# Optimization experiments

Hardware: AMD Instinct MI355X
Metric: run time of the kernel (lower is better)

Reference implementation:

```python
import jax, jax.numpy as jnp
import numpy as np

H = 8
D_MODEL = 512
D_K = D_MODEL // H
NEG = -1e9


def setup_inputs() -> dict:
    key = jax.random.key(0)
    ks = jax.random.split(key, 12)
    N, Lq, Lk = 2, 4096, 4096
    inp = {
        "query": jax.random.normal(ks[0], (N, Lq, D_MODEL), dtype=jnp.float32),
        "key": jax.random.normal(ks[1], (N, Lk, D_MODEL), dtype=jnp.float32),
        "value": jax.random.normal(ks[2], (N, Lk, D_MODEL), dtype=jnp.float32),
        "mask": jnp.ones((N, 1, Lk), dtype=jnp.int32),
    }
    scale = 0.02
    for i, nm in enumerate(["q", "k", "v", "o"]):
        inp[f"W{nm}"] = scale * jax.random.normal(ks[3 + i], (D_MODEL, D_MODEL), dtype=jnp.float32)
        inp[f"b{nm}"] = jnp.zeros((D_MODEL,), dtype=jnp.float32)
    return inp


def reference(query, key, value, mask, Wq, bq, Wk, bk, Wv, bv, Wo, bo):
    # torch Linear: y = x @ W.T + b
    N, Lq, _ = query.shape
    Lk = key.shape[1]
    q = (query @ Wq.T + bq).reshape(N, Lq, H, D_K)   # (N,Lq,h,dk)
    k = (key @ Wk.T + bk).reshape(N, Lk, H, D_K)     # (N,Lk,h,dk)
    v = (value @ Wv.T + bv).reshape(N, Lk, H, D_K)   # (N,Lk,h,dk)
    # scores: (N,h,Lq,Lk)
    scores = jnp.einsum("bqhd,bkhd->bhqk", q, k) / jnp.sqrt(jnp.float32(D_K))
    # mask (N,1,Lk) or (N,Lq,Lk) -> broadcast over heads (and Lq if singleton)
    m = mask[:, None, :, :]  # (N,1,1|Lq,Lk)
    scores = jnp.where(m == 0, jnp.float32(NEG), scores)
    attn = jax.nn.softmax(scores, axis=-1)
    # dropout is identity in eval mode (deterministic reference)
    out = jnp.einsum("bhqk,bkhd->bqhd", attn, v).reshape(N, Lq, D_MODEL)
    return out @ Wo.T + bo
```

## Files before the change

### kernel.cpp

```cpp
#include <hip/hip_runtime.h>
#include <hip/hip_bf16.h>

#define H 8
#define DM 512
#define DK 64
#define LSEQ 4096
#define NB 2
#define NSPLIT 4
#define KSPAN (LSEQ / NSPLIT)
#define NIT (KSPAN / 64)

#define QSCALE 0.18033688011112042f

typedef float f32x4 __attribute__((ext_vector_type(4)));
typedef __bf16 bf16x8 __attribute__((ext_vector_type(8)));
typedef __bf16 bf16x2 __attribute__((ext_vector_type(2)));
typedef unsigned short u16;

__device__ __forceinline__ u16 f2bf(float f) {
    union { float f; unsigned u; } v{f};
    return (u16)((v.u + 0x8000u) >> 16);
}

__device__ __forceinline__ unsigned pkbf(float a, float b) {
#if __has_builtin(__builtin_amdgcn_cvt_pk_bf16_f32)
    union { bf16x2 v; unsigned u; } x;
    x.v = __builtin_amdgcn_cvt_pk_bf16_f32(a, b);
    return x.u;
#else
    union { float f; unsigned u; } x{a}, y{b};
    return ((x.u + 0x8000u) >> 16) | ((y.u + 0x8000u) & 0xffff0000u);
#endif
}

__device__ __forceinline__ ushort4 cvt4(float4 a) {
    union { ushort4 s; uint2 u; } o;
    o.u.x = pkbf(a.x, a.y);
    o.u.y = pkbf(a.z, a.w);
    return o.s;
}

__device__ __forceinline__ float2 ubf2(unsigned u) {
    union { float f; unsigned v; } a, b;
    a.v = u << 16;
    b.v = u & 0xffff0000u;
    return make_float2(a.f, b.f);
}

__device__ __forceinline__ float fexp2(float x) {
#if __has_builtin(__builtin_amdgcn_exp2f)
    return __builtin_amdgcn_exp2f(x);
#else
    return exp2f(x);
#endif
}

__device__ __forceinline__ f32x4 mfma32(bf16x8 a, bf16x8 b, f32x4 c) {
    return __builtin_amdgcn_mfma_f32_16x16x32_bf16(a, b, c, 0, 0, 0);
}

__launch_bounds__(256, 2)
__global__ void proj_qkv(const float* __restrict__ Xq, const float* __restrict__ Xk,
                         const float* __restrict__ Xv,
                         const float* __restrict__ Wq, const float* __restrict__ Wk,
                         const float* __restrict__ Wv,
                         const float* __restrict__ bq, const float* __restrict__ bk,
                         const float* __restrict__ bv,
                         const int* __restrict__ mask,
                         u16* __restrict__ qo, u16* __restrict__ ko, u16* __restrict__ vo)
{
    const int mode = blockIdx.z;
    const float* X    = (mode == 0) ? Xq : (mode == 1) ? Xk : Xv;
    const float* W    = (mode == 0) ? Wq : (mode == 1) ? Wk : Wv;
    const float* bias = (mode == 0) ? bq : (mode == 1) ? bk : bv;
    u16* out          = (mode == 0) ? qo : (mode == 1) ? ko : vo;

    __shared__ __align__(16) u16 As[2][128][72];
    __shared__ __align__(16) u16 Bs[2][128][72];

    const int tid  = threadIdx.x;
    const int wave = tid >> 6;
    const int lane = tid & 63;
    const int g    = lane >> 4;
    const int ln   = lane & 15;
    const int wr   = wave >> 1;
    const int wc   = wave & 1;

    const int m0 = blockIdx.x * 128;
    const int n0 = blockIdx.y * 128;

    float4 xa[8], wb[8];
    #pragma unroll
    for (int i = 0; i < 8; ++i) {
        int idx = tid + 256 * i;
        int row = idx >> 4;
        int col = (idx & 15) * 4;
        xa[i] = *(const float4*)(X + (size_t)(m0 + row) * DM + col);
        wb[i] = *(const float4*)(W + (size_t)(n0 + row) * DM + col);
    }
    #pragma unroll
    for (int i = 0; i < 8; ++i) {
        int idx = tid + 256 * i;
        int row = idx >> 4;
        int col = (idx & 15) * 4;
        *(ushort4*)&As[0][row][col] = cvt4(xa[i]);
        *(ushort4*)&Bs[0][row][col] = cvt4(wb[i]);
    }

    f32x4 acc[4][4] = {};

    for (int kt = 0; kt < 8; ++kt) {
        const int cur = kt & 1;
        __syncthreads();

        if (kt < 7) {
            int kb = (kt + 1) * 64;
            #pragma unroll
            for (int i = 0; i < 8; ++i) {
                int idx = tid + 256 * i;
                int row = idx >> 4;
                int col = (idx & 15) * 4;
                xa[i] = *(const float4*)(X + (size_t)(m0 + row) * DM + kb + col);
                wb[i] = *(const float4*)(W + (size_t)(n0 + row) * DM + kb + col);
            }
        }

        bf16x8 af[4][2], bf[4][2];
        #pragma unroll
        for (int t = 0; t < 4; ++t) {
            af[t][0] = *(const bf16x8*)&As[cur][wr * 64 + t * 16 + ln][g * 8];
            af[t][1] = *(const bf16x8*)&As[cur][wr * 64 + t * 16 + ln][32 + g * 8];
            bf[t][0] = *(const bf16x8*)&Bs[cur][wc * 64 + t * 16 + ln][g * 8];
            bf[t][1] = *(const bf16x8*)&Bs[cur][wc * 64 + t * 16 + ln][32 + g * 8];
        }
        #pragma unroll
        for (int mt = 0; mt < 4; ++mt)
            #pragma unroll
            for (int nt = 0; nt < 4; ++nt) {
                acc[mt][nt] = mfma32(af[mt][0], bf[nt][0], acc[mt][nt]);
                acc[mt][nt] = mfma32(af[mt][1], bf[nt][1], acc[mt][nt]);
            }

        if (kt < 7) {
            int nxt = 1 - cur;
            #pragma unroll
            for (int i = 0; i < 8; ++i) {
                int idx = tid + 256 * i;
                int row = idx >> 4;
                int col = (idx & 15) * 4;
                *(ushort4*)&As[nxt][row][col] = cvt4(xa[i]);
                *(ushort4*)&Bs[nxt][row][col] = cvt4(wb[i]);
            }
        }
    }

    if (mode != 2) {
        #pragma unroll
        for (int nt = 0; nt < 4; ++nt) {
            int n  = n0 + wc * 64 + nt * 16 + ln;
            float bias_n = bias[n];
            int hh = n >> 6;
            int d  = n & (DK - 1);
            #pragma unroll
            for (int mt = 0; mt < 4; ++mt)
                #pragma unroll
                for (int r = 0; r < 4; ++r) {
                    int m  = m0 + wr * 64 + mt * 16 + g * 4 + r;
                    int bb = m >> 12;
                    int s  = m & (LSEQ - 1);
                    float val = acc[mt][nt][r] + bias_n;
                    if (mode == 0) val *= QSCALE;
                    else           val = mask[bb * LSEQ + s] ? val : 0.0f;
                    out[(size_t)((bb * H + hh) * LSEQ + s) * DK + d] = f2bf(val);
                }
        }
    } else {
        __syncthreads();
        u16* Ts = &As[0][0][0];
        const int bb = m0 >> 12;
        const int s0 = m0 & (LSEQ - 1);
        #pragma unroll
        for (int nt = 0; nt < 4; ++nt) {
            int dl = wc * 64 + nt * 16 + ln;
            float bias_n = bias[n0 + dl];
            #pragma unroll
            for (int mt = 0; mt < 4; ++mt)
                #pragma unroll
                for (int r = 0; r < 4; ++r) {
                    int sl = wr * 64 + mt * 16 + g * 4 + r;
                    float val = acc[mt][nt][r] + bias_n;
                    val = mask[bb * LSEQ + s0 + sl] ? val : 0.0f;
                    Ts[dl * 136 + sl] = f2bf(val);
                }
        }
        __syncthreads();
        int dl   = tid >> 1;
        int half = tid & 1;
        int n  = n0 + dl;
        int hh = n >> 6;
        int d  = n & (DK - 1);
        int sb = s0 + half * 64;
        u16* dst = out + ((size_t)((bb * H + hh) * DK + d) * LSEQ + sb);
        const u16* srcp = Ts + dl * 136 + half * 64;
        #pragma unroll
        for (int i = 0; i < 8; ++i)
            *(uint4*)(dst + i * 8) = *(const uint4*)(srcp + i * 8);
    }
}

__launch_bounds__(256, 4)
__global__ void flash(const u16* __restrict__ qws, const u16* __restrict__ kws,
                      const u16* __restrict__ vws, const int* __restrict__ mask,
                      u16* __restrict__ Opart, float* __restrict__ lpart)
{
    __shared__ u16 Ks[2][64][64];
    __shared__ u16 Vs[2][64][64];

    const int tid   = threadIdx.x;
    const int wave  = tid >> 6;
    const int lane  = tid & 63;
    const int g     = lane >> 4;
    const int ln    = lane & 15;
    const int b     = blockIdx.z;
    const int h     = blockIdx.y;
    const int qblk  = blockIdx.x & 31;
    const int split = blockIdx.x >> 5;
    const int q0    = qblk * 128;
    const int kstart = split * KSPAN;

    const u16* qp = qws + ((size_t)((b * H + h) * LSEQ) + q0 + wave * 32 + ln) * DK;
    const u16* kp = kws + (size_t)(b * H + h) * LSEQ * DK;
    const u16* vp = vws + (size_t)(b * H + h) * DK * LSEQ;
    const int* mp = mask + b * LSEQ;

    int nmask = 0;
    for (int t = 0; t < NIT; ++t) {
        int mval = mp[kstart + t * 64 + lane];
        unsigned long long bal = __ballot(mval == 0);
        nmask += (int)__popcll(bal);
    }
    const float fnmask = (float)nmask;

    bf16x8 qf[2][2];
    qf[0][0] = *(const bf16x8*)(qp + g * 8);
    qf[0][1] = *(const bf16x8*)(qp + 32 + g * 8);
    qf[1][0] = *(const bf16x8*)(qp + 16 * DK + g * 8);
    qf[1][1] = *(const bf16x8*)(qp + 16 * DK + 32 + g * 8);

    union OU { unsigned u[4]; bf16x8 v; } onesu;
    onesu.u[0] = onesu.u[1] = onesu.u[2] = onesu.u[3] = 0x3F803F80u;
    const bf16x8 vones = onesu.v;

    f32x4 accO[2][4] = {};
    f32x4 accL[2] = {};
    const f32x4 fzero = {};

    const int row = tid >> 3;
    const int c   = tid & 7;
    const int swz = row & 7;
    const int kcol = (c ^ swz) * 8;
    const int vcol0 = ((2 * c) & 3) * 16 + (c >> 1) * 4;
    const int vs0 = vcol0 >> 3;
    const int vof = vcol0 & 7;
    const int vw0 = ((vs0 ^ swz) * 8) + vof;
    const int vw1 = (((vs0 + 2) ^ swz) * 8) + vof;
    const int rs = ln & 7;

    uint4 kr0, kr1, vr0, vr1;
    kr0 = *(const uint4*)(kp + (size_t)(kstart + row) * DK + c * 8);
    kr1 = *(const uint4*)(kp + (size_t)(kstart + row + 32) * DK + c * 8);
    vr0 = *(const uint4*)(vp + (size_t)row * LSEQ + kstart + c * 8);
    vr1 = *(const uint4*)(vp + (size_t)(row + 32) * LSEQ + kstart + c * 8);
    *(uint4*)&Ks[0][row][kcol]      = kr0;
    *(uint4*)&Ks[0][row + 32][kcol] = kr1;
    *(uint2*)&Vs[0][row][vw0]       = make_uint2(vr0.x, vr0.y);
    *(uint2*)&Vs[0][row][vw1]       = make_uint2(vr0.z, vr0.w);
    *(uint2*)&Vs[0][row + 32][vw0]  = make_uint2(vr1.x, vr1.y);
    *(uint2*)&Vs[0][row + 32][vw1]  = make_uint2(vr1.z, vr1.w);

    for (int it = 0; it < NIT; ++it) {
        const int cur = it & 1;
        __syncthreads();

        if (it < NIT - 1) {
            int kn = kstart + it * 64 + 64;
            kr0 = *(const uint4*)(kp + (size_t)(kn + row) * DK + c * 8);
            kr1 = *(const uint4*)(kp + (size_t)(kn + row + 32) * DK + c * 8);
            vr0 = *(const uint4*)(vp + (size_t)row * LSEQ + kn + c * 8);
            vr1 = *(const uint4*)(vp + (size_t)(row + 32) * LSEQ + kn + c * 8);
        }

        __builtin_amdgcn_s_setprio(1);
        f32x4 sc[2][4];
        #pragma unroll
        for (int kb = 0; kb < 4; ++kb) {
            bf16x8 kf0 = *(const bf16x8*)&Ks[cur][kb * 16 + ln][(g ^ rs) * 8];
            bf16x8 kf1 = *(const bf16x8*)&Ks[cur][kb * 16 + ln][((g + 4) ^ rs) * 8];
            #pragma unroll
            for (int j = 0; j < 2; ++j) {
                f32x4 z = mfma32(kf0, qf[j][0], fzero);
                z = mfma32(kf1, qf[j][1], z);
                sc[j][kb] = z;
            }
        }
        __builtin_amdgcn_s_setprio(0);

        #pragma unroll
        for (int kb = 0; kb < 4; ++kb)
            #pragma unroll
            for (int j = 0; j < 2; ++j) {
                sc[j][kb][0] = fexp2(sc[j][kb][0]);
                sc[j][kb][1] = fexp2(sc[j][kb][1]);
                sc[j][kb][2] = fexp2(sc[j][kb][2]);
                sc[j][kb][3] = fexp2(sc[j][kb][3]);
            }

        union PU { unsigned u[4]; bf16x8 v; } p01[2], p23[2];
        #pragma unroll
        for (int j = 0; j < 2; ++j) {
            p01[j].u[0] = pkbf(sc[j][0][0], sc[j][0][1]);
            p01[j].u[1] = pkbf(sc[j][0][2], sc[j][0][3]);
            p01[j].u[2] = pkbf(sc[j][1][0], sc[j][1][1]);
            p01[j].u[3] = pkbf(sc[j][1][2], sc[j][1][3]);
            p23[j].u[0] = pkbf(sc[j][2][0], sc[j][2][1]);
            p23[j].u[1] = pkbf(sc[j][2][2], sc[j][2][3]);
            p23[j].u[2] = pkbf(sc[j][3][0], sc[j][3][1]);
            p23[j].u[3] = pkbf(sc[j][3][2], sc[j][3][3]);
        }

        __builtin_amdgcn_s_setprio(1);
        #pragma unroll
        for (int j = 0; j < 2; ++j) {
            accL[j] = mfma32(p01[j].v, vones, accL[j]);
            accL[j] = mfma32(p23[j].v, vones, accL[j]);
        }
        #pragma unroll
        for (int t = 0; t < 4; ++t) {
            bf16x8 vb01 = *(const bf16x8*)&Vs[cur][t * 16 + ln][((2 * g) ^ rs) * 8];
            bf16x8 vb23 = *(const bf16x8*)&Vs[cur][t * 16 + ln][((2 * g + 1) ^ rs) * 8];
            #pragma unroll
            for (int j = 0; j < 2; ++j) {
                accO[j][t] = mfma32(p01[j].v, vb01, accO[j][t]);
                accO[j][t] = mfma32(p23[j].v, vb23, accO[j][t]);
            }
        }
        __builtin_amdgcn_s_setprio(0);

        if (it < NIT - 1) {
            int nxt = 1 - cur;
            *(uint4*)&Ks[nxt][row][kcol]      = kr0;
            *(uint4*)&Ks[nxt][row + 32][kcol] = kr1;
            *(uint2*)&Vs[nxt][row][vw0]       = make_uint2(vr0.x, vr0.y);
            *(uint2*)&Vs[nxt][row][vw1]       = make_uint2(vr0.z, vr0.w);
            *(uint2*)&Vs[nxt][row + 32][vw0]  = make_uint2(vr1.x, vr1.y);
            *(uint2*)&Vs[nxt][row + 32][vw1]  = make_uint2(vr1.z, vr1.w);
        }
    }

    const size_t PLANE = (size_t)NB * LSEQ * DM;
    u16* opp = Opart + (size_t)split * PLANE;

    #pragma unroll
    for (int j = 0; j < 2; ++j) {
        if (ln == 0) {
            #pragma unroll
            for (int r = 0; r < 4; ++r)
                lpart[(size_t)split * (NB * H * LSEQ) + ((size_t)(b * H + h) * LSEQ)
                      + q0 + wave * 32 + j * 16 + g * 4 + r] = accL[j][r] - fnmask;
        }
        #pragma unroll
        for (int r = 0; r < 4; ++r) {
            float linv = 1.0f / (accL[j][r] - fnmask);
            size_t base = ((size_t)(b * LSEQ) + q0 + wave * 32 + j * 16 + g * 4 + r) * DM + h * DK;
            #pragma unroll
            for (int t = 0; t < 4; ++t)
                opp[base + t * 16 + ln] = f2bf(accO[j][t][r] * linv);
        }
    }
}

__launch_bounds__(256, 4)
__global__ void reduce_split(const u16* __restrict__ Opart, const float* __restrict__ lpart,
                             u16* __restrict__ ows)
{
    const size_t PLANE = (size_t)NB * LSEQ * DM;
    const size_t LP    = (size_t)NB * H * LSEQ;
    size_t gid  = (size_t)blockIdx.x * 256 + threadIdx.x;
    size_t flat = gid * 8;

    int b   = (int)(flat >> 21);
    int rem = (int)(flat & ((1 << 21) - 1));
    int q   = rem >> 9;
    int hh  = (rem & 511) >> 6;
    size_t lidx = ((size_t)(b * H + hh) * LSEQ) + q;

    float ls[NSPLIT];
    float lsum = 0.0f;
    #pragma unroll
    for (int s = 0; s < NSPLIT; ++s) {
        ls[s] = lpart[(size_t)s * LP + lidx];
        lsum += ls[s];
    }
    float inv = 1.0f / lsum;

    float o[8] = {};
    #pragma unroll
    for (int s = 0; s < NSPLIT; ++s) {
        float w = ls[s] * inv;
        uint4 cc = *(const uint4*)(Opart + (size_t)s * PLANE + flat);
        float2 a;
        a = ubf2(cc.x); o[0] += w * a.x; o[1] += w * a.y;
        a = ubf2(cc.y); o[2] += w * a.x; o[3] += w * a.y;
        a = ubf2(cc.z); o[4] += w * a.x; o[5] += w * a.y;
        a = ubf2(cc.w); o[6] += w * a.x; o[7] += w * a.y;
    }
    uint4 r;
    r.x = pkbf(o[0], o[1]);
    r.y = pkbf(o[2], o[3]);
    r.z = pkbf(o[4], o[5]);
    r.w = pkbf(o[6], o[7]);
    *(uint4*)(ows + flat) = r;
}

__launch_bounds__(256, 3)
__global__ void proj_out(const u16* __restrict__ A, const float* __restrict__ Wo,
                         const float* __restrict__ bo, float* __restrict__ out)
{
    __shared__ __align__(16) u16 As[2][128][68];
    __shared__ __align__(16) u16 Bs[2][64][68];

    const int tid  = threadIdx.x;
    const int wave = tid >> 6;
    const int lane = tid & 63;
    const int g    = lane >> 4;
    const int ln   = lane & 15;

    const int m0 = blockIdx.x * 128;
    const int n0 = blockIdx.y * 64;

    uint4 aa[4];
    float4 wb[4];
    #pragma unroll
    for (int i = 0; i < 4; ++i) {
        int idx = tid + 256 * i;
        int row = idx >> 3;
        int col = (idx & 7) * 8;
        aa[i] = *(const uint4*)(A + (size_t)(m0 + row) * DM + col);
        int rwb = idx >> 4;
        int cwb = (idx & 15) * 4;
        wb[i] = *(const float4*)(Wo + (size_t)(n0 + rwb) * DM + cwb);
    }
    #pragma unroll
    for (int i = 0; i < 4; ++i) {
        int idx = tid + 256 * i;
        int row = idx >> 3;
        int col = (idx & 7) * 8;
        *(uint4*)&As[0][row][col] = aa[i];
        int rwb = idx >> 4;
        int cwb = (idx & 15) * 4;
        *(ushort4*)&Bs[0][rwb][cwb] = cvt4(wb[i]);
    }

    f32x4 acc[2][4] = {};

    for (int kt = 0; kt < 8; ++kt) {
        const int cur = kt & 1;
        __syncthreads();

        if (kt < 7) {
            int kb = (kt + 1) * 64;
            #pragma unroll
            for (int i = 0; i < 4; ++i) {
                int idx = tid + 256 * i;
                int row = idx >> 3;
                int col = (idx & 7) * 8;
                aa[i] = *(const uint4*)(A + (size_t)(m0 + row) * DM + kb + col);
                int rwb = idx >> 4;
                int cwb = (idx & 15) * 4;
                wb[i] = *(const float4*)(Wo + (size_t)(n0 + rwb) * DM + kb + cwb);
            }
        }

        bf16x8 af[2][2], bf[4][2];
        #pragma unroll
        for (int mt = 0; mt < 2; ++mt) {
            af[mt][0] = *(const bf16x8*)&As[cur][wave * 32 + mt * 16 + ln][g * 8];
            af[mt][1] = *(const bf16x8*)&As[cur][wave * 32 + mt * 16 + ln][32 + g * 8];
        }
        #pragma unroll
        for (int nt = 0; nt < 4; ++nt) {
            bf[nt][0] = *(const bf16x8*)&Bs[cur][nt * 16 + ln][g * 8];
            bf[nt][1] = *(const bf16x8*)&Bs[cur][nt * 16 + ln][32 + g * 8];
        }
        #pragma unroll
        for (int mt = 0; mt < 2; ++mt)
            #pragma unroll
            for (int nt = 0; nt < 4; ++nt) {
                acc[mt][nt] = mfma32(af[mt][0], bf[nt][0], acc[mt][nt]);
                acc[mt][nt] = mfma32(af[mt][1], bf[nt][1], acc[mt][nt]);
            }

        if (kt < 7) {
            int nxt = 1 - cur;
            #pragma unroll
            for (int i = 0; i < 4; ++i) {
                int idx = tid + 256 * i;
                int row = idx >> 3;
                int col = (idx & 7) * 8;
                *(uint4*)&As[nxt][row][col] = aa[i];
                int rwb = idx >> 4;
                int cwb = (idx & 15) * 4;
                *(ushort4*)&Bs[nxt][rwb][cwb] = cvt4(wb[i]);
            }
        }
    }

    #pragma unroll
    for (int nt = 0; nt < 4; ++nt) {
        int n = n0 + nt * 16 + ln;
        float bias_n = bo[n];
        #pragma unroll
        for (int mt = 0; mt < 2; ++mt)
            #pragma unroll
            for (int r = 0; r < 4; ++r) {
                int m = m0 + wave * 32 + mt * 16 + g * 4 + r;
                out[(size_t)m * DM + n] = acc[mt][nt][r] + bias_n;
            }
    }
}

extern "C" void kernel_launch(void* const* d_in, const int* in_sizes, int n_in,
                              void* d_out, int out_size, void* d_ws, size_t ws_size,
                              hipStream_t stream) {
    (void)in_sizes; (void)n_in; (void)out_size; (void)ws_size;

    const float* query = (const float*)d_in[0];
    const float* key   = (const float*)d_in[1];
    const float* value = (const float*)d_in[2];
    const int*   mask  = (const int*)d_in[3];
    const float* Wq = (const float*)d_in[4];
    const float* bq = (const float*)d_in[5];
    const float* Wk = (const float*)d_in[6];
    const float* bk = (const float*)d_in[7];
    const float* Wv = (const float*)d_in[8];
    const float* bv = (const float*)d_in[9];
    const float* Wo = (const float*)d_in[10];
    const float* bo = (const float*)d_in[11];
    float* out = (float*)d_out;

    const size_t PLANE = (size_t)NB * H * LSEQ * DK;
    u16* qws   = (u16*)d_ws;
    u16* kws   = qws + PLANE;
    u16* vws   = kws + PLANE;
    u16* ows   = vws + PLANE;
    u16* Opart = ows + PLANE;
    float* lpart = (float*)(Opart + (size_t)NSPLIT * PLANE);

    dim3 blk(256);
    proj_qkv<<<dim3(64, 4, 3), blk, 0, stream>>>(query, key, value, Wq, Wk, Wv,
                                                 bq, bk, bv, mask, qws, kws, vws);
    flash<<<dim3(32 * NSPLIT, H, NB), blk, 0, stream>>>(qws, kws, vws, mask, Opart, lpart);
    reduce_split<<<dim3(2048), blk, 0, stream>>>(Opart, lpart, ows);
    proj_out<<<dim3(64, 8, 1), blk, 0, stream>>>(ows, Wo, bo, out);
}
```

Before: 231.5 us.

## Fuse split-K softmax combine into output projection A-tile loads

Removes the separate reduce_split kernel and performs the weighted combination of the four partial attention outputs inside proj_out while loading A tiles. This eliminates one kernel launch and the write/read of the intermediate combined buffer. In exchange, each output-projection block re-reads all four partial planes and recomputes the combine, and this is repeated across the column-block grid dimension. The reciprocal is also switched to a fast hardware rcp.

```diff
diff --git a/kernel.cpp b/kernel.cpp
--- a/kernel.cpp
+++ b/kernel.cpp
@@ -45,6 +45,14 @@
     a.v = u << 16;
     b.v = u & 0xffff0000u;
     return make_float2(a.f, b.f);
+}
+
+__device__ __forceinline__ float frcp(float x) {
+#if __has_builtin(__builtin_amdgcn_rcpf)
+    return __builtin_amdgcn_rcpf(x);
+#else
+    return 1.0f / x;
+#endif
 }
 
 __device__ __forceinline__ float fexp2(float x) {
@@ -379,51 +387,59 @@
     }
 }
 
-__launch_bounds__(256, 4)
-__global__ void reduce_split(const u16* __restrict__ Opart, const float* __restrict__ lpart,
-                             u16* __restrict__ ows)
+__device__ __forceinline__ uint4 combine4(const u16* __restrict__ Opart,
+                                          const float* __restrict__ lpart,
+                                          int m, int kcol)
 {
     const size_t PLANE = (size_t)NB * LSEQ * DM;
     const size_t LP    = (size_t)NB * H * LSEQ;
-    size_t gid  = (size_t)blockIdx.x * 256 + threadIdx.x;
-    size_t flat = gid * 8;
-
-    int b   = (int)(flat >> 21);
-    int rem = (int)(flat & ((1 << 21) - 1));
-    int q   = rem >> 9;
-    int hh  = (rem & 511) >> 6;
-    size_t lidx = ((size_t)(b * H + hh) * LSEQ) + q;
-
-    float ls[NSPLIT];
-    float lsum = 0.0f;
-    #pragma unroll
-    for (int s = 0; s < NSPLIT; ++s) {
-        ls[s] = lpart[(size_t)s * LP + lidx];
-        lsum += ls[s];
-    }
-    float inv = 1.0f / lsum;
-
-    float o[8] = {};
-    #pragma unroll
-    for (int s = 0; s < NSPLIT; ++s) {
-        float w = ls[s] * inv;
-        uint4 cc = *(const uint4*)(Opart + (size_t)s * PLANE + flat);
-        float2 a;
-        a = ubf2(cc.x); o[0] += w * a.x; o[1] += w * a.y;
-        a = ubf2(cc.y); o[2] += w * a.x; o[3] += w * a.y;
-        a = ubf2(cc.z); o[4] += w * a.x; o[5] += w * a.y;
-        a = ubf2(cc.w); o[6] += w * a.x; o[7] += w * a.y;
-    }
+    const int b  = m >> 12;
+    const int q  = m & (LSEQ - 1);
+    const int hh = kcol >> 6;
+    const size_t lidx = ((size_t)(b * H + hh) * LSEQ) + q;
+    float l0 = lpart[lidx];
+    float l1 = lpart[LP + lidx];
+    float l2 = lpart[2 * LP + lidx];
+    float l3 = lpart[3 * LP + lidx];
+    float inv = frcp(l0 + l1 + l2 + l3);
+    float w0 = l0 * inv, w1 = l1 * inv, w2 = l2 * inv, w3 = l3 * inv;
+
+    const size_t fi = (size_t)m * DM + kcol;
+    uint4 c0 = *(const uint4*)(Opart + fi);
+    uint4 c1 = *(const uint4*)(Opart + PLANE + fi);
+    uint4 c2 = *(const uint4*)(Opart + 2 * PLANE + fi);
+    uint4 c3 = *(const uint4*)(Opart + 3 * PLANE + fi);
+
+    float o0, o1, o2, o3, o4, o5, o6, o7;
+    float2 a;
+    a = ubf2(c0.x); o0  = w0 * a.x; o1  = w0 * a.y;
+    a = ubf2(c0.y); o2  = w0 * a.x; o3  = w0 * a.y;
+    a = ubf2(c0.z); o4  = w0 * a.x; o5  = w0 * a.y;
+    a = ubf2(c0.w); o6  = w0 * a.x; o7  = w0 * a.y;
+    a = ubf2(c1.x); o0 += w1 * a.x; o1 += w1 * a.y;
+    a = ubf2(c1.y); o2 += w1 * a.x; o3 += w1 * a.y;
+    a = ubf2(c1.z); o4 += w1 * a.x; o5 += w1 * a.y;
+    a = ubf2(c1.w); o6 += w1 * a.x; o7 += w1 * a.y;
+    a = ubf2(c2.x); o0 += w2 * a.x; o1 += w2 * a.y;
+    a = ubf2(c2.y); o2 += w2 * a.x; o3 += w2 * a.y;
+    a = ubf2(c2.z); o4 += w2 * a.x; o5 += w2 * a.y;
+    a = ubf2(c2.w); o6 += w2 * a.x; o7 += w2 * a.y;
+    a = ubf2(c3.x); o0 += w3 * a.x; o1 += w3 * a.y;
+    a = ubf2(c3.y); o2 += w3 * a.x; o3 += w3 * a.y;
+    a = ubf2(c3.z); o4 += w3 * a.x; o5 += w3 * a.y;
+    a = ubf2(c3.w); o6 += w3 * a.x; o7 += w3 * a.y;
+
     uint4 r;
-    r.x = pkbf(o[0], o[1]);
-    r.y = pkbf(o[2], o[3]);
-    r.z = pkbf(o[4], o[5]);
-    r.w = pkbf(o[6], o[7]);
-    *(uint4*)(ows + flat) = r;
+    r.x = pkbf(o0, o1);
+    r.y = pkbf(o2, o3);
+    r.z = pkbf(o4, o5);
+    r.w = pkbf(o6, o7);
+    return r;
 }
 
 __launch_bounds__(256, 3)
-__global__ void proj_out(const u16* __restrict__ A, const float* __restrict__ Wo,
+__global__ void proj_out(const u16* __restrict__ Opart, const float* __restrict__ lpart,
+                         const float* __restrict__ Wo,
                          const float* __restrict__ bo, float* __restrict__ out)
 {
     __shared__ __align__(16) u16 As[2][128][68];
@@ -445,7 +461,7 @@
         int idx = tid + 256 * i;
         int row = idx >> 3;
         int col = (idx & 7) * 8;
-        aa[i] = *(const uint4*)(A + (size_t)(m0 + row) * DM + col);
+        aa[i] = combine4(Opart, lpart, m0 + row, col);
         int rwb = idx >> 4;
         int cwb = (idx & 15) * 4;
         wb[i] = *(const float4*)(Wo + (size_t)(n0 + rwb) * DM + cwb);
@@ -474,7 +490,7 @@
                 int idx = tid + 256 * i;
                 int row = idx >> 3;
                 int col = (idx & 7) * 8;
-                aa[i] = *(const uint4*)(A + (size_t)(m0 + row) * DM + kb + col);
+                aa[i] = combine4(Opart, lpart, m0 + row, kb + col);
                 int rwb = idx >> 4;
                 int cwb = (idx & 15) * 4;
                 wb[i] = *(const float4*)(Wo + (size_t)(n0 + rwb) * DM + kb + cwb);
@@ -560,6 +576,5 @@
     proj_qkv<<<dim3(64, 4, 3), blk, 0, stream>>>(query, key, value, Wq, Wk, Wv,
                                                  bq, bk, bv, mask, qws, kws, vws);
     flash<<<dim3(32 * NSPLIT, H, NB), blk, 0, stream>>>(qws, kws, vws, mask, Opart, lpart);
-    reduce_split<<<dim3(2048), blk, 0, stream>>>(Opart, lpart, ows);
-    proj_out<<<dim3(64, 8, 1), blk, 0, stream>>>(ows, Wo, bo, out);
-}
+    proj_out<<<dim3(64, 8, 1), blk, 0, stream>>>(Opart, lpart, Wo, bo, out);
+}
```

Measured after the change: 255.1 us. 10.2% more time.

## Pre-convert inputs and weights to bf16 in a separate pass, shrink GEMM K-tiles

Applied to the files above, without the earlier changes.

A new cvt_all kernel converts the four weight matrices and the three activation inputs from fp32 to bf16 once, writing them into workspace that reuses the Opart region. proj_qkv and proj_out then load bf16 directly, with K-tile 32 instead of 64, smaller LDS footprints and higher occupancy bounds. The aim is to stop the GEMM tiles from reconverting the same fp32 data many times and to halve their global load volume. The cost is an extra kernel launch plus a full read and write pass over the inputs, and twice as many K-loop iterations and barriers.

```diff
diff --git a/kernel.cpp b/kernel.cpp
--- a/kernel.cpp
+++ b/kernel.cpp
@@ -59,24 +59,51 @@
     return __builtin_amdgcn_mfma_f32_16x16x32_bf16(a, b, c, 0, 0, 0);
 }
 
-__launch_bounds__(256, 2)
-__global__ void proj_qkv(const float* __restrict__ Xq, const float* __restrict__ Xk,
-                         const float* __restrict__ Xv,
-                         const float* __restrict__ Wq, const float* __restrict__ Wk,
-                         const float* __restrict__ Wv,
+__launch_bounds__(256, 8)
+__global__ void cvt_all(const float* __restrict__ W0, const float* __restrict__ W1,
+                        const float* __restrict__ W2, const float* __restrict__ W3,
+                        const float* __restrict__ X0, const float* __restrict__ X1,
+                        const float* __restrict__ X2,
+                        u16* __restrict__ wout, u16* __restrict__ xout)
+{
+    const int y = blockIdx.y;
+    const float* src;
+    u16* dst;
+    int nblk;
+    if (y < 4) {
+        src = (y == 0) ? W0 : (y == 1) ? W1 : (y == 2) ? W2 : W3;
+        dst = wout + (size_t)y * DM * DM;
+        nblk = (DM * DM) / (256 * 8);
+    } else {
+        src = (y == 4) ? X0 : (y == 5) ? X1 : X2;
+        dst = xout + (size_t)(y - 4) * ((size_t)NB * LSEQ * DM);
+        nblk = ((size_t)NB * LSEQ * DM) / (256 * 8);
+    }
+    if ((int)blockIdx.x >= nblk) return;
+    size_t base = ((size_t)blockIdx.x * 256 + threadIdx.x) * 8;
+    float4 a = *(const float4*)(src + base);
+    float4 b = *(const float4*)(src + base + 4);
+    *(ushort4*)(dst + base)     = cvt4(a);
+    *(ushort4*)(dst + base + 4) = cvt4(b);
+}
+
+__launch_bounds__(256, 3)
+__global__ void proj_qkv(const u16* __restrict__ xbf,
+                         const u16* __restrict__ wbf,
                          const float* __restrict__ bq, const float* __restrict__ bk,
                          const float* __restrict__ bv,
                          const int* __restrict__ mask,
                          u16* __restrict__ qo, u16* __restrict__ ko, u16* __restrict__ vo)
 {
     const int mode = blockIdx.z;
-    const float* X    = (mode == 0) ? Xq : (mode == 1) ? Xk : Xv;
-    const float* W    = (mode == 0) ? Wq : (mode == 1) ? Wk : Wv;
+    const u16* X      = xbf + (size_t)mode * ((size_t)NB * LSEQ * DM);
+    const u16* Wb     = wbf + (size_t)mode * DM * DM;
     const float* bias = (mode == 0) ? bq : (mode == 1) ? bk : bv;
     u16* out          = (mode == 0) ? qo : (mode == 1) ? ko : vo;
 
-    __shared__ __align__(16) u16 As[2][128][72];
-    __shared__ __align__(16) u16 Bs[2][128][72];
+    __shared__ __align__(16) u16 sbuf[2][2][128][40];
+    u16 (*As)[128][40] = sbuf[0];
+    u16 (*Bs)[128][40] = sbuf[1];
 
     const int tid  = threadIdx.x;
     const int wave = tid >> 6;
@@ -89,67 +116,63 @@
     const int m0 = blockIdx.x * 128;
     const int n0 = blockIdx.y * 128;
 
-    float4 xa[8], wb[8];
-    #pragma unroll
-    for (int i = 0; i < 8; ++i) {
+    uint4 xa[2], wa[2];
+    #pragma unroll
+    for (int i = 0; i < 2; ++i) {
         int idx = tid + 256 * i;
-        int row = idx >> 4;
-        int col = (idx & 15) * 4;
-        xa[i] = *(const float4*)(X + (size_t)(m0 + row) * DM + col);
-        wb[i] = *(const float4*)(W + (size_t)(n0 + row) * DM + col);
-    }
-    #pragma unroll
-    for (int i = 0; i < 8; ++i) {
+        int row = idx >> 2;
+        int col = (idx & 3) * 8;
+        xa[i] = *(const uint4*)(X  + (size_t)(m0 + row) * DM + col);
+        wa[i] = *(const uint4*)(Wb + (size_t)(n0 + row) * DM + col);
+    }
+    #pragma unroll
+    for (int i = 0; i < 2; ++i) {
         int idx = tid + 256 * i;
-        int row = idx >> 4;
-        int col = (idx & 15) * 4;
-        *(ushort4*)&As[0][row][col] = cvt4(xa[i]);
-        *(ushort4*)&Bs[0][row][col] = cvt4(wb[i]);
+        int row = idx >> 2;
+        int col = (idx & 3) * 8;
+        *(uint4*)&As[0][row][col] = xa[i];
+        *(uint4*)&Bs[0][row][col] = wa[i];
     }
 
     f32x4 acc[4][4] = {};
 
-    for (int kt = 0; kt < 8; ++kt) {
+    for (int kt = 0; kt < 16; ++kt) {
         const int cur = kt & 1;
         __syncthreads();
 
-        if (kt < 7) {
-            int kb = (kt + 1) * 64;
-            #pragma unroll
-            for (int i = 0; i < 8; ++i) {
+        if (kt < 15) {
+            int kb = (kt + 1) * 32;
+            #pragma unroll
+            for (int i = 0; i < 2; ++i) {
                 int idx = tid + 256 * i;
-                int row = idx >> 4;
-                int col = (idx & 15) * 4;
-                xa[i] = *(const float4*)(X + (size_t)(m0 + row) * DM + kb + col);
-                wb[i] = *(const float4*)(W + (size_t)(n0 + row) * DM + kb + col);
-            }
-        }
-
-        bf16x8 af[4][2], bf[4][2];
+                int row = idx >> 2;
+                int col = (idx & 3) * 8;
+                xa[i] = *(const uint4*)(X  + (size_t)(m0 + row) * DM + kb + col);
+                wa[i] = *(const uint4*)(Wb + (size_t)(n0 + row) * DM + kb + col);
+            }
+        }
+
+        bf16x8 af[4], bf[4];
         #pragma unroll
         for (int t = 0; t < 4; ++t) {
-            af[t][0] = *(const bf16x8*)&As[cur][wr * 64 + t * 16 + ln][g * 8];
-            af[t][1] = *(const bf16x8*)&As[cur][wr * 64 + t * 16 + ln][32 + g * 8];
-            bf[t][0] = *(const bf16x8*)&Bs[cur][wc * 64 + t * 16 + ln][g * 8];
-            bf[t][1] = *(const bf16x8*)&Bs[cur][wc * 64 + t * 16 + ln][32 + g * 8];
+            af[t] = *(const bf16x8*)&As[cur][wr * 64 + t * 16 + ln][g * 8];
+            bf[t] = *(const bf16x8*)&Bs[cur][wc * 64 + t * 16 + ln][g * 8];
         }
         #pragma unroll
         for (int mt = 0; mt < 4; ++mt)
             #pragma unroll
-            for (int nt = 0; nt < 4; ++nt) {
-                acc[mt][nt] = mfma32(af[mt][0], bf[nt][0], acc[mt][nt]);
-                acc[mt][nt] = mfma32(af[mt][1], bf[nt][1], acc[mt][nt]);
-            }
-
-        if (kt < 7) {
+            for (int nt = 0; nt < 4; ++nt)
+                acc[mt][nt] = mfma32(af[mt], bf[nt], acc[mt][nt]);
+
+        if (kt < 15) {
             int nxt = 1 - cur;
             #pragma unroll
-            for (int i = 0; i < 8; ++i) {
+            for (int i = 0; i < 2; ++i) {
                 int idx = tid + 256 * i;
-                int row = idx >> 4;
-                int col = (idx & 15) * 4;
-                *(ushort4*)&As[nxt][row][col] = cvt4(xa[i]);
-                *(ushort4*)&Bs[nxt][row][col] = cvt4(wb[i]);
+                int row = idx >> 2;
+                int col = (idx & 3) * 8;
+                *(uint4*)&As[nxt][row][col] = xa[i];
+                *(uint4*)&Bs[nxt][row][col] = wa[i];
             }
         }
     }
@@ -176,7 +199,7 @@
         }
     } else {
         __syncthreads();
-        u16* Ts = &As[0][0][0];
+        u16* Ts = &sbuf[0][0][0][0];
         const int bb = m0 >> 12;
         const int s0 = m0 & (LSEQ - 1);
         #pragma unroll
@@ -422,12 +445,12 @@
     *(uint4*)(ows + flat) = r;
 }
 
-__launch_bounds__(256, 3)
-__global__ void proj_out(const u16* __restrict__ A, const float* __restrict__ Wo,
+__launch_bounds__(256, 4)
+__global__ void proj_out(const u16* __restrict__ A, const u16* __restrict__ Wob,
                          const float* __restrict__ bo, float* __restrict__ out)
 {
-    __shared__ __align__(16) u16 As[2][128][68];
-    __shared__ __align__(16) u16 Bs[2][64][68];
+    __shared__ __align__(16) u16 As2[2][128][40];
+    __shared__ __align__(16) u16 Bs2[2][64][40];
 
     const int tid  = threadIdx.x;
     const int wave = tid >> 6;
@@ -438,80 +461,77 @@
     const int m0 = blockIdx.x * 128;
     const int n0 = blockIdx.y * 64;
 
-    uint4 aa[4];
-    float4 wb[4];
-    #pragma unroll
-    for (int i = 0; i < 4; ++i) {
+    uint4 aa[2], wa;
+    #pragma unroll
+    for (int i = 0; i < 2; ++i) {
         int idx = tid + 256 * i;
-        int row = idx >> 3;
-        int col = (idx & 7) * 8;
+        int row = idx >> 2;
+        int col = (idx & 3) * 8;
         aa[i] = *(const uint4*)(A + (size_t)(m0 + row) * DM + col);
-        int rwb = idx >> 4;
-        int cwb = (idx & 15) * 4;
-        wb[i] = *(const float4*)(Wo + (size_t)(n0 + rwb) * DM + cwb);
-    }
-    #pragma unroll
-    for (int i = 0; i < 4; ++i) {
+    }
+    {
+        int row = tid >> 2;
+        int col = (tid & 3) * 8;
+        wa = *(const uint4*)(Wob + (size_t)(n0 + row) * DM + col);
+    }
+    #pragma unroll
+    for (int i = 0; i < 2; ++i) {
         int idx = tid + 256 * i;
-        int row = idx >> 3;
-        int col = (idx & 7) * 8;
-        *(uint4*)&As[0][row][col] = aa[i];
-        int rwb = idx >> 4;
-        int cwb = (idx & 15) * 4;
-        *(ushort4*)&Bs[0][rwb][cwb] = cvt4(wb[i]);
+        int row = idx >> 2;
+        int col = (idx & 3) * 8;
+        *(uint4*)&As2[0][row][col] = aa[i];
+    }
+    {
+        int row = tid >> 2;
+        int col = (tid & 3) * 8;
+        *(uint4*)&Bs2[0][row][col] = wa;
     }
 
     f32x4 acc[2][4] = {};
 
-    for (int kt = 0; kt < 8; ++kt) {
+    for (int kt = 0; kt < 16; ++kt) {
         const int cur = kt & 1;
         __syncthreads();
 
-        if (kt < 7) {
-            int kb = (kt + 1) * 64;
-            #pragma unroll
-            for (int i = 0; i < 4; ++i) {
+        if (kt < 15) {
+            int kb = (kt + 1) * 32;
+            #pragma unroll
+            for (int i = 0; i < 2; ++i) {
                 int idx = tid + 256 * i;
-                int row = idx >> 3;
-                int col = (idx & 7) * 8;
+                int row = idx >> 2;
+                int col = (idx & 3) * 8;
                 aa[i] = *(const uint4*)(A + (size_t)(m0 + row) * DM + kb + col);
-                int rwb = idx >> 4;
-                int cwb = (idx & 15) * 4;
-                wb[i] = *(const float4*)(Wo + (size_t)(n0 + rwb) * DM + kb + cwb);
-            }
-        }
-
-        bf16x8 af[2][2], bf[4][2];
-        #pragma unroll
-        for (int mt = 0; mt < 2; ++mt) {
-            af[mt][0] = *(const bf16x8*)&As[cur][wave * 32 + mt * 16 + ln][g * 8];
-            af[mt][1] = *(const bf16x8*)&As[cur][wave * 32 + mt * 16 + ln][32 + g * 8];
-        }
-        #pragma unroll
-        for (int nt = 0; nt < 4; ++nt) {
-            bf[nt][0] = *(const bf16x8*)&Bs[cur][nt * 16 + ln][g * 8];
-            bf[nt][1] = *(const bf16x8*)&Bs[cur][nt * 16 + ln][32 + g * 8];
-        }
+            }
+            int row = tid >> 2;
+            int col = (tid & 3) * 8;
+            wa = *(const uint4*)(Wob + (size_t)(n0 + row) * DM + kb + col);
+        }
+
+        bf16x8 af[2], bf[4];
         #pragma unroll
         for (int mt = 0; mt < 2; ++mt)
-            #pragma unroll
-            for (int nt = 0; nt < 4; ++nt) {
-                acc[mt][nt] = mfma32(af[mt][0], bf[nt][0], acc[mt][nt]);
-                acc[mt][nt] = mfma32(af[mt][1], bf[nt][1], acc[mt][nt]);
-            }
-
-        if (kt < 7) {
+            af[mt] = *(const bf16x8*)&As2[cur][wave * 32 + mt * 16 + ln][g * 8];
+        #pragma unroll
+        for (int nt = 0; nt < 4; ++nt)
+            bf[nt] = *(const bf16x8*)&Bs2[cur][nt * 16 + ln][g * 8];
+        #pragma unroll
+        for (int mt = 0; mt < 2; ++mt)
+            #pragma unroll
+            for (int nt = 0; nt < 4; ++nt)
+                acc[mt][nt] = mfma32(af[mt], bf[nt], acc[mt][nt]);
+
+        if (kt < 15) {
             int nxt = 1 - cur;
             #pragma unroll
-            for (int i = 0; i < 4; ++i) {
+            for (int i = 0; i < 2; ++i) {
                 int idx = tid + 256 * i;
-                int row = idx >> 3;
-                int col = (idx & 7) * 8;
-                *(uint4*)&As[nxt][row][col] = aa[i];
-                int rwb = idx >> 4;
-                int cwb = (idx & 15) * 4;
-                *(ushort4*)&Bs[nxt][rwb][cwb] = cvt4(wb[i]);
-            }
+                int row = idx >> 2;
+                int col = (idx & 3) * 8;
+                *(uint4*)&As2[nxt][row][col] = aa[i];
+            }
+            int row = tid >> 2;
+            int col = (tid & 3) * 8;
+            *(uint4*)&Bs2[nxt][row][col] = wa;
         }
     }
 
@@ -555,11 +575,15 @@
     u16* ows   = vws + PLANE;
     u16* Opart = ows + PLANE;
     float* lpart = (float*)(Opart + (size_t)NSPLIT * PLANE);
+    u16* wbf   = (u16*)(lpart + (size_t)NSPLIT * NB * H * LSEQ);
+    u16* xbf   = Opart;
 
     dim3 blk(256);
-    proj_qkv<<<dim3(64, 4, 3), blk, 0, stream>>>(query, key, value, Wq, Wk, Wv,
-                                                 bq, bk, bv, mask, qws, kws, vws);
+    cvt_all<<<dim3(2048, 7), blk, 0, stream>>>(Wq, Wk, Wv, Wo, query, key, value,
+                                               wbf, xbf);
+    proj_qkv<<<dim3(64, 4, 3), blk, 0, stream>>>(xbf, wbf, bq, bk, bv, mask,
+                                                 qws, kws, vws);
     flash<<<dim3(32 * NSPLIT, H, NB), blk, 0, stream>>>(qws, kws, vws, mask, Opart, lpart);
     reduce_split<<<dim3(2048), blk, 0, stream>>>(Opart, lpart, ows);
-    proj_out<<<dim3(64, 8, 1), blk, 0, stream>>>(ows, Wo, bo, out);
-}
+    proj_out<<<dim3(64, 8, 1), blk, 0, stream>>>(ows, wbf + 3 * (size_t)DM * DM, bo, out);
+}
```

After: 238.0 us. +2.8%, slower.
